# Kernel optimization log

Hardware: AMD Instinct MI355X
Metric: run time of the kernel (lower is better)

## Reference

```python
import jax, jax.numpy as jnp
import numpy as np

DIM = 2048
N_HEADS = 16
HEAD_DIM = DIM // N_HEADS        # 128
HALF_HD = HEAD_DIM // 2          # 64 (per-context per-head dim)
Q_DIM = DIM // 2                 # 1024
KV_DIM = DIM // 2                # 1024 (n_kv_heads == n_heads)
TOTAL = Q_DIM + 2 * KV_DIM       # 3072
B, S = 2, 2048
EPS = 1e-5


def rmsnorm(x, w, eps=EPS):
    return x * jax.lax.rsqrt(jnp.mean(x * x, axis=-1, keepdims=True) + eps) * w


def rope(x, freqs):
    # x: [B,S,H,D] with D even; freqs: [S, D//2] angles
    xr = x[..., 0::2]
    xi = x[..., 1::2]
    cos = jnp.cos(freqs)[None, :, None, :]
    sin = jnp.sin(freqs)[None, :, None, :]
    out_r = xr * cos - xi * sin
    out_i = xr * sin + xi * cos
    return jnp.stack([out_r, out_i], axis=-1).reshape(x.shape)


def setup_inputs() -> dict:
    key = jax.random.key(0)
    ks = jax.random.split(key, 10)
    inp = {
        "local_c": jax.random.normal(ks[0], (B, S, DIM), jnp.float32),
        "global_c": jax.random.normal(ks[1], (B, S, DIM), jnp.float32),
        "freqs": jax.random.uniform(ks[2], (S, HALF_HD // 2), jnp.float32) * 6.28,
        "W_lc": jax.random.normal(ks[3], (TOTAL, DIM), jnp.float32) * 0.02,
        "W_gc": jax.random.normal(ks[4], (TOTAL, DIM), jnp.float32) * 0.02,
        "q_lc_nw": jnp.ones((Q_DIM,), jnp.float32),
        "k_lc_nw": jnp.ones((KV_DIM,), jnp.float32),
        "q_gc_nw": jnp.ones((Q_DIM,), jnp.float32),
        "k_gc_nw": jnp.ones((KV_DIM,), jnp.float32),
        "q_cat_nw": jnp.ones((HEAD_DIM,), jnp.float32),
        "k_cat_nw": jnp.ones((HEAD_DIM,), jnp.float32),
        "W_lo": jax.random.normal(ks[5], (DIM, 2 * Q_DIM), jnp.float32) * 0.02,
        "b_lo": jnp.zeros((DIM,), jnp.float32),
        "lc_on_w": jnp.ones((DIM,), jnp.float32),
        "W_go": jax.random.normal(ks[6], (DIM, 2 * Q_DIM), jnp.float32) * 0.02,
        "b_go": jnp.zeros((DIM,), jnp.float32),
        "gc_on_w": jnp.ones((DIM,), jnp.float32),
    }
    return inp


def _context_build(x, W, q_nw, k_nw):
    comb = jnp.einsum('bsd,td->bst', x, W)
    q, k, v = jnp.split(comb, [Q_DIM, Q_DIM + KV_DIM], axis=-1)
    q = rmsnorm(q, q_nw).reshape(B, S, N_HEADS, HALF_HD)
    k = rmsnorm(k, k_nw).reshape(B, S, N_HEADS, HALF_HD)
    v = v.reshape(B, S, N_HEADS, HALF_HD)
    return q, k, v


def reference(local_c, global_c, freqs, W_lc, W_gc, q_lc_nw, k_lc_nw, q_gc_nw,
              k_gc_nw, q_cat_nw, k_cat_nw, W_lo, b_lo, lc_on_w, W_go, b_go, gc_on_w):
    q_lc, k_lc, v_lc = _context_build(local_c, W_lc, q_lc_nw, k_lc_nw)
    q_gc, k_gc, v_gc = _context_build(global_c, W_gc, q_gc_nw, k_gc_nw)

    q_lc = rope(q_lc, freqs)
    k_lc = rope(k_lc, freqs)
    q_gc = rope(q_gc, freqs)
    k_gc = rope(k_gc, freqs)

    # concat local+global per head -> [B,S,H,HEAD_DIM], QK-norm over head dim
    xq = rmsnorm(jnp.concatenate([q_lc, q_gc], axis=-1), q_cat_nw)
    xk = rmsnorm(jnp.concatenate([k_lc, k_gc], axis=-1), k_cat_nw)
    xv = jnp.concatenate([v_lc, v_gc], axis=-1)

    scale = 1.0 / np.sqrt(HEAD_DIM)
    scores = jnp.einsum('bqhd,bkhd->bhqk', xq, xk) * scale
    attn = jax.nn.softmax(scores, axis=-1)
    out = jnp.einsum('bhqk,bkhd->bqhd', attn, xv).reshape(B, S, DIM)

    x_lc = rmsnorm(jnp.einsum('bsd,od->bso', out, W_lo) + b_lo, lc_on_w)
    x_gc = rmsnorm(jnp.einsum('bsd,od->bso', out, W_go) + b_go, gc_on_w)
    return (x_lc, x_gc)
```

## Files before the change

### kernel.cpp

```cpp
#include <hip/hip_runtime.h>
#include <hip/hip_bf16.h>

#define DIM 2048
#define NH 16
#define HD 128
#define QD 1024
#define TOT 3072
#define BB 2
#define SS 2048
#define NTOK (BB*SS)
#define EPS 1e-5f

typedef __attribute__((ext_vector_type(4))) float f32x4;
typedef __attribute__((ext_vector_type(8))) short short8;
typedef __attribute__((ext_vector_type(8))) unsigned short u16x8;
typedef __attribute__((ext_vector_type(4))) unsigned short u16x4;

__device__ __forceinline__ float b2f(unsigned short u){
    unsigned int x = ((unsigned int)u) << 16;
    return __builtin_bit_cast(float, x);
}
__device__ __forceinline__ unsigned short f2b(float f){
    unsigned int x = __builtin_bit_cast(unsigned int, f);
    x = (x + 0x7fffu + ((x >> 16) & 1u)) >> 16;
    return (unsigned short)x;
}
__device__ __forceinline__ float exp2_fast(float x){
    float r;
    asm("v_exp_f32 %0, %1" : "=v"(r) : "v"(x));
    return r;
}
__device__ __forceinline__ void store_c(float* p, float v){ *p = v; }
__device__ __forceinline__ void store_c(unsigned short* p, float v){ *p = f2b(v); }

#define MFMA16(a,b,c) __builtin_amdgcn_mfma_f32_16x16x32_bf16((a),(b),(c),0,0,0)

#define GLOAD16(g, l) __builtin_amdgcn_global_load_lds( \
    (const __attribute__((address_space(1))) unsigned int*)(g), \
    (__attribute__((address_space(3))) unsigned int*)(l), 16, 0, 0)

__device__ __forceinline__ void cvt8(const float* __restrict__ s,
                                     unsigned short* __restrict__ d, int i){
    const float4* p = reinterpret_cast<const float4*>(s + (size_t)i * 8);
    float4 a = p[0], b = p[1];
    u16x8 o;
    o[0]=f2b(a.x); o[1]=f2b(a.y); o[2]=f2b(a.z); o[3]=f2b(a.w);
    o[4]=f2b(b.x); o[5]=f2b(b.y); o[6]=f2b(b.z); o[7]=f2b(b.w);
    *reinterpret_cast<u16x8*>(d + (size_t)i * 8) = o;
}

__global__ __launch_bounds__(256) void cvt_multi(
    const float* __restrict__ s0, const float* __restrict__ s1,
    const float* __restrict__ s2, const float* __restrict__ s3,
    const float* __restrict__ s4, const float* __restrict__ s5,
    unsigned short* __restrict__ d0, unsigned short* __restrict__ d1,
    unsigned short* __restrict__ d2, unsigned short* __restrict__ d3,
    unsigned short* __restrict__ d4, unsigned short* __restrict__ d5)
{
    const int N0 = NTOK*DIM/8;
    const int N1 = N0 + NTOK*DIM/8;
    const int N2 = N1 + TOT*DIM/8;
    const int N3 = N2 + TOT*DIM/8;
    const int N4 = N3 + DIM*DIM/8;
    const int N5 = N4 + DIM*DIM/8;
    for (int i = blockIdx.x * blockDim.x + threadIdx.x; i < N5;
         i += gridDim.x * blockDim.x){
        if      (i < N0) cvt8(s0, d0, i);
        else if (i < N1) cvt8(s1, d1, i - N0);
        else if (i < N2) cvt8(s2, d2, i - N1);
        else if (i < N3) cvt8(s3, d3, i - N2);
        else if (i < N4) cvt8(s4, d4, i - N3);
        else             cvt8(s5, d5, i - N4);
    }
}

template<typename OutT>
__global__ __launch_bounds__(256) void gemm_nt(const unsigned short* __restrict__ A0,
                                               const unsigned short* __restrict__ B0,
                                               OutT* __restrict__ C0,
                                               const unsigned short* __restrict__ A1,
                                               const unsigned short* __restrict__ B1,
                                               OutT* __restrict__ C1,
                                               int M, int N, int K){
    __shared__ __attribute__((aligned(16))) unsigned short As[2][128*64];
    __shared__ __attribute__((aligned(16))) unsigned short Bs[3][128*64];
    const int t = threadIdx.x;
    const int lane = t & 63;
    const int w = t >> 6;
    const int wr = w >> 1, wc = w & 1;
    const int gx = gridDim.x;
    const int nwg = gx * gridDim.y;
    int zsel, swz;
    if (gridDim.z == 2){
        const int glin = (int)(blockIdx.z * nwg + blockIdx.y * gx + blockIdx.x);
        const int xcd = glin & 7;
        const int i = glin >> 3;
        zsel = xcd >> 2;
        swz = (xcd & 3) * (nwg >> 2) + i;
    } else {
        const int lin = (int)(blockIdx.y * gx + blockIdx.x);
        const int cpx = nwg >> 3;
        swz = (lin & 7) * cpx + (lin >> 3);
        zsel = 0;
    }
    const unsigned short* A = zsel ? A1 : A0;
    const unsigned short* B = zsel ? B1 : B0;
    OutT* C = zsel ? C1 : C0;
    const int m0 = (swz / gx) * 128, n0 = (swz % gx) * 128;
    const int l16 = lane & 15, lq = lane >> 4;

    f32x4 acc[4][4];
    const f32x4 z = {0.f, 0.f, 0.f, 0.f};
    #pragma unroll
    for (int m = 0; m < 4; ++m)
        #pragma unroll
        for (int n = 0; n < 4; ++n) acc[m][n] = z;

    auto stageA = [&](int kt, int bi){
        #pragma unroll
        for (int i = 0; i < 4; ++i){
            int c = t + 256 * i;
            int row = c >> 3, c8 = c & 7;
            int cg = (c8 ^ (row & 7)) * 8;
            GLOAD16(&A[(size_t)(m0 + row) * K + kt*64 + cg],
                    (char*)&As[bi][0] + (size_t)(i * 256 + w * 64) * 16);
        }
    };
    auto stageB = [&](int kt, int bi){
        #pragma unroll
        for (int i = 0; i < 4; ++i){
            int c = t + 256 * i;
            int row = c >> 3, c8 = c & 7;
            int cg = (c8 ^ (row & 7)) * 8;
            GLOAD16(&B[(size_t)(n0 + row) * K + kt*64 + cg],
                    (char*)&Bs[bi][0] + (size_t)(i * 256 + w * 64) * 16);
        }
    };

    const int NTt = K >> 6;
    stageA(0, 0); stageB(0, 0);
    if (NTt > 1) stageB(1, 1);
    if (NTt > 1) asm volatile("s_waitcnt vmcnt(4)" ::: "memory");
    else         asm volatile("s_waitcnt vmcnt(0)" ::: "memory");
    __builtin_amdgcn_s_barrier();
    __builtin_amdgcn_sched_barrier(0);

    int a0 = 0, b0 = 0, b1 = 1, b2 = 2;
    for (int kt = 0; kt < NTt; ++kt){
        if (kt + 1 < NTt) stageA(kt + 1, a0 ^ 1);
        if (kt + 2 < NTt) stageB(kt + 2, b2);
        #pragma unroll
        for (int kk = 0; kk < 2; ++kk){
            short8 af[4], bf[4];
            #pragma unroll
            for (int m = 0; m < 4; ++m){
                int row = wr*64 + m*16 + l16;
                af[m] = *reinterpret_cast<const short8*>(
                    &As[a0][row*64 + (((kk*4 + lq) ^ (row & 7)) * 8)]);
            }
            #pragma unroll
            for (int n = 0; n < 4; ++n){
                int row = wc*64 + n*16 + l16;
                bf[n] = *reinterpret_cast<const short8*>(
                    &Bs[b0][row*64 + (((kk*4 + lq) ^ (row & 7)) * 8)]);
            }
            #pragma unroll
            for (int m = 0; m < 4; ++m)
                #pragma unroll
                for (int n = 0; n < 4; ++n)
                    acc[m][n] = MFMA16(af[m], bf[n], acc[m][n]);
        }
        if (kt + 1 < NTt){
            if (kt + 2 < NTt) asm volatile("s_waitcnt vmcnt(4)" ::: "memory");
            else              asm volatile("s_waitcnt vmcnt(0)" ::: "memory");
            __builtin_amdgcn_s_barrier();
            __builtin_amdgcn_sched_barrier(0);
        }
        a0 ^= 1;
        int tmp = b0; b0 = b1; b1 = b2; b2 = tmp;
    }
    #pragma unroll
    for (int m = 0; m < 4; ++m){
        int grow = m0 + wr*64 + m*16 + lq*4;
        #pragma unroll
        for (int n = 0; n < 4; ++n){
            int gcol = n0 + wc*64 + n*16 + l16;
            #pragma unroll
            for (int r = 0; r < 4; ++r)
                store_c(&C[(size_t)(grow + r) * N + gcol], acc[m][n][r]);
        }
    }
}

__global__ __launch_bounds__(256) void qkv_post(
    const unsigned short* __restrict__ comb_lc, const unsigned short* __restrict__ comb_gc,
    const float* __restrict__ freqs,
    const float* __restrict__ q_lc_nw, const float* __restrict__ k_lc_nw,
    const float* __restrict__ q_gc_nw, const float* __restrict__ k_gc_nw,
    const float* __restrict__ q_cat_nw, const float* __restrict__ k_cat_nw,
    unsigned short* __restrict__ xq, unsigned short* __restrict__ xk,
    unsigned short* __restrict__ xv)
{
    __shared__ float qcat[16][128];
    __shared__ float kcat[16][128];
    __shared__ float rbuf[4][4];
    const int tok = blockIdx.x;
    const int s = tok & (SS - 1);
    const unsigned short* clc = comb_lc + (size_t)tok * TOT;
    const unsigned short* cgc = comb_gc + (size_t)tok * TOT;
    const int t = threadIdx.x;
    const int lane = t & 63, w = t >> 6;

    const unsigned short* segs[4] = { clc, clc + QD, cgc, cgc + QD };
    const float* wts[4] = { q_lc_nw, k_lc_nw, q_gc_nw, k_gc_nw };

    float ss4[4];
    #pragma unroll
    for (int sg = 0; sg < 4; ++sg){
        u16x4 v = *reinterpret_cast<const u16x4*>(segs[sg] + t * 4);
        float acc = 0.f;
        #pragma unroll
        for (int j = 0; j < 4; ++j){ float f = b2f(v[j]); acc += f * f; }
        ss4[sg] = acc;
    }
    #pragma unroll
    for (int sg = 0; sg < 4; ++sg){
        float v = ss4[sg];
        #pragma unroll
        for (int o = 32; o >= 1; o >>= 1) v += __shfl_xor(v, o);
        if (lane == 0) rbuf[sg][w] = v;
    }
    __syncthreads();
    float rms[4];
    #pragma unroll
    for (int sg = 0; sg < 4; ++sg){
        float tot = rbuf[sg][0] + rbuf[sg][1] + rbuf[sg][2] + rbuf[sg][3];
        rms[sg] = rsqrtf(tot * (1.f / QD) + EPS);
    }

    #pragma unroll
    for (int sg = 0; sg < 4; ++sg){
        const unsigned short* seg = segs[sg];
        const float* wt = wts[sg];
        const float rf = rms[sg];
        float (*dst)[128] = (sg == 0 || sg == 2) ? qcat : kcat;
        const int coff = (sg >= 2) ? 64 : 0;
        #pragma unroll
        for (int pi = 0; pi < 2; ++pi){
            int p = t + pi * 256;
            int h = p >> 5, j = p & 31;
            int idx = h * 64 + 2 * j;
            float xr = b2f(seg[idx])     * rf * wt[idx];
            float xi = b2f(seg[idx + 1]) * rf * wt[idx + 1];
            float fr = freqs[(size_t)s * 32 + j];
            float cs = __cosf(fr), sn = __sinf(fr);
            dst[h][coff + 2*j]     = xr * cs - xi * sn;
            dst[h][coff + 2*j + 1] = xr * sn + xi * cs;
        }
    }

    {
        int i0 = t * 4;
        int h = i0 >> 6, d = i0 & 63;
        u16x4 vlc = *reinterpret_cast<const u16x4*>(clc + 2048 + i0);
        u16x4 vgc = *reinterpret_cast<const u16x4*>(cgc + 2048 + i0);
        *reinterpret_cast<u16x4*>(&xv[(size_t)tok * DIM + h * 128 + d])      = vlc;
        *reinterpret_cast<u16x4*>(&xv[(size_t)tok * DIM + h * 128 + 64 + d]) = vgc;
    }
    __syncthreads();

    {
        int h = t >> 4, sub = t & 15;
        float sq = 0.f, sk = 0.f;
        #pragma unroll
        for (int j = 0; j < 8; ++j){
            float a = qcat[h][sub*8 + j]; sq += a * a;
            float b = kcat[h][sub*8 + j]; sk += b * b;
        }
        #pragma unroll
        for (int o = 1; o < 16; o <<= 1){ sq += __shfl_xor(sq, o); sk += __shfl_xor(sk, o); }
        float rq = rsqrtf(sq * (1.f / 128) + EPS);
        float rk = rsqrtf(sk * (1.f / 128) + EPS);
        u16x8 oq, ok;
        #pragma unroll
        for (int j = 0; j < 8; ++j){
            int d = sub*8 + j;
            oq[j] = f2b(qcat[h][d] * rq * q_cat_nw[d]);
            ok[j] = f2b(kcat[h][d] * rk * k_cat_nw[d]);
        }
        *reinterpret_cast<u16x8*>(&xq[(size_t)tok * DIM + h * 128 + sub*8]) = oq;
        *reinterpret_cast<u16x8*>(&xk[(size_t)tok * DIM + h * 128 + sub*8]) = ok;
    }
}

__global__ __launch_bounds__(256) void transpose_v(const unsigned short* __restrict__ xv,
                                                   unsigned short* __restrict__ xvT){
    __shared__ unsigned short tile[128][129];
    const int blk = blockIdx.x;
    const int st = blk & 15;
    const int bh = blk >> 4;
    const int b = bh >> 4, h = bh & 15;
    const int t = threadIdx.x;
    const int s0 = st * 128;
    #pragma unroll
    for (int i = 0; i < 8; ++i){
        int c = t + 256 * i;
        int r = c >> 4, dc = c & 15;
        u16x8 v = *reinterpret_cast<const u16x8*>(&xv[((size_t)(b*SS + s0 + r)) * DIM + h*HD + dc*8]);
        #pragma unroll
        for (int j = 0; j < 8; ++j) tile[r][dc*8 + j] = v[j];
    }
    __syncthreads();
    #pragma unroll
    for (int i = 0; i < 8; ++i){
        int c = t + 256 * i;
        int d = c >> 4, sc = c & 15;
        u16x8 o;
        #pragma unroll
        for (int j = 0; j < 8; ++j) o[j] = tile[sc*8 + j][d];
        *reinterpret_cast<u16x8*>(&xvT[((size_t)bh * HD + d) * SS + s0 + sc*8]) = o;
    }
}

__global__ __launch_bounds__(256) void attn_fwd(const unsigned short* __restrict__ xq,
                                                const unsigned short* __restrict__ xk,
                                                const unsigned short* __restrict__ xvT,
                                                unsigned short* __restrict__ attn_out){
    __shared__ __attribute__((aligned(16))) unsigned short Kl[2][64 * 128];
    __shared__ __attribute__((aligned(16))) unsigned short Vt[2][128 * 64];
    __shared__ __attribute__((aligned(16))) unsigned short Pl[4][2][16 * 64];
    const int blk = ((int)blockIdx.x & 7) * 64 + ((int)blockIdx.x >> 3);
    const int qt = blk & 15, h = (blk >> 4) & 15, b = blk >> 8;
    const int t = threadIdx.x, lane = t & 63, w = t >> 6;
    const int l16 = lane & 15, lq = lane >> 4;
    const float scale2 = 0.12751744751f;
    const float MBIAS = 16.6f;
    const int qbase = qt * 128 + w * 32;

    short8 qf[2][4];
    #pragma unroll
    for (int g = 0; g < 2; ++g)
        #pragma unroll
        for (int ks = 0; ks < 4; ++ks)
            qf[g][ks] = *reinterpret_cast<const short8*>(
                &xq[((size_t)(b*SS + qbase + g*16 + l16)) * DIM + h*HD + ks*32 + lq*8]);

    float psum[2] = {0.f, 0.f};
    f32x4 O[2][8];
    const f32x4 z = {0.f, 0.f, 0.f, 0.f};
    #pragma unroll
    for (int g = 0; g < 2; ++g)
        #pragma unroll
        for (int dn = 0; dn < 8; ++dn) O[g][dn] = z;

    const size_t kbase = (size_t)(b*SS) * DIM + h*HD;
    const size_t vbase = ((size_t)(b*NH + h)) * HD * SS;

    auto stage = [&](int kt, int bi){
        #pragma unroll
        for (int i = 0; i < 4; ++i){
            int slot = i*256 + w*64 + lane;
            int r = slot >> 4, dc = slot & 15;
            GLOAD16(&xk[kbase + (size_t)(kt*64 + r) * DIM + ((dc ^ (r & 7)) * 8)],
                    (char*)&Kl[bi][0] + (size_t)(i*256 + w*64) * 16);
            int d = slot >> 3, kc = slot & 7;
            GLOAD16(&xvT[vbase + (size_t)d * SS + kt*64 + ((kc ^ (d & 7)) * 8)],
                    (char*)&Vt[bi][0] + (size_t)(i*256 + w*64) * 16);
        }
    };

    stage(0, 0);
    __syncthreads();

    int cur = 0;

    for (int kt = 0; kt < SS/64; ++kt){
        if (kt + 1 < SS/64) stage(kt + 1, cur ^ 1);

        const unsigned short* Kc = Kl[cur];
        const unsigned short* Vc = Vt[cur];

        #pragma unroll
        for (int g = 0; g < 2; ++g){
            f32x4 St[4];
            #pragma unroll
            for (int kn = 0; kn < 4; ++kn) St[kn] = z;
            __builtin_amdgcn_s_setprio(1);
            #pragma unroll
            for (int kn = 0; kn < 4; ++kn){
                int kr = kn*16 + l16;
                #pragma unroll
                for (int ks = 0; ks < 4; ++ks){
                    short8 ak = *reinterpret_cast<const short8*>(
                        &Kc[kr*128 + (((ks*4 + lq) ^ (kr & 7)) * 8)]);
                    St[kn] = MFMA16(ak, qf[g][ks], St[kn]);
                }
            }
            __builtin_amdgcn_s_setprio(0);

            unsigned short* P = Pl[w][g];
            #pragma unroll
            for (int kn = 0; kn < 4; ++kn){
                float p0 = exp2_fast(St[kn][0]*scale2 - MBIAS);
                float p1 = exp2_fast(St[kn][1]*scale2 - MBIAS);
                float p2 = exp2_fast(St[kn][2]*scale2 - MBIAS);
                float p3 = exp2_fast(St[kn][3]*scale2 - MBIAS);
                psum[g] += (p0 + p1) + (p2 + p3);
                unsigned lo, hi;
                asm("v_cvt_pk_bf16_f32 %0, %1, %2" : "=v"(lo) : "v"(p0), "v"(p1));
                asm("v_cvt_pk_bf16_f32 %0, %1, %2" : "=v"(hi) : "v"(p2), "v"(p3));
                uint2 pk2; pk2.x = lo; pk2.y = hi;
                int kk = kn >> 1;
                int lqp = (kn & 1)*2 + (lq >> 1);
                *reinterpret_cast<uint2*>(&P[(kk*64 + lqp*16 + l16)*8 + (lq & 1)*4]) = pk2;
            }
        }
        asm volatile("s_waitcnt lgkmcnt(0)" ::: "memory");
        __builtin_amdgcn_sched_barrier(0);

        __builtin_amdgcn_s_setprio(1);
        #pragma unroll
        for (int kk = 0; kk < 2; ++kk){
            short8 pb0 = *reinterpret_cast<const short8*>(&Pl[w][0][(kk*64 + lq*16 + l16)*8]);
            short8 pb1 = *reinterpret_cast<const short8*>(&Pl[w][1][(kk*64 + lq*16 + l16)*8]);
            #pragma unroll
            for (int dn = 0; dn < 8; ++dn){
                int dr = dn*16 + l16;
                short8 av = *reinterpret_cast<const short8*>(
                    &Vc[dr*64 + (((kk*4 + lq) ^ (dr & 7)) * 8)]);
                O[0][dn] = MFMA16(av, pb0, O[0][dn]);
                O[1][dn] = MFMA16(av, pb1, O[1][dn]);
            }
        }
        __builtin_amdgcn_s_setprio(0);

        __syncthreads();
        cur ^= 1;
    }

    #pragma unroll
    for (int g = 0; g < 2; ++g){
        float ps = psum[g];
        ps += __shfl_xor(ps, 16);
        ps += __shfl_xor(ps, 32);
        float inv = 1.f / ps;
        #pragma unroll
        for (int dn = 0; dn < 8; ++dn){
            u16x4 o4;
            #pragma unroll
            for (int r = 0; r < 4; ++r) o4[r] = f2b(O[g][dn][r] * inv);
            *reinterpret_cast<u16x4*>(
                &attn_out[((size_t)(b*SS + qbase + g*16 + l16)) * DIM + h*HD + dn*16 + lq*4]) = o4;
        }
    }
}

__global__ __launch_bounds__(256) void proj_norm2(const unsigned short* __restrict__ proj,
                                                  const float* __restrict__ b_lo,
                                                  const float* __restrict__ b_go,
                                                  const float* __restrict__ w_lc,
                                                  const float* __restrict__ w_gc,
                                                  float* __restrict__ out){
    __shared__ float buf[DIM];
    __shared__ float rbuf[4];
    const int half = blockIdx.x >> 12;
    const int row  = blockIdx.x & (NTOK - 1);
    const unsigned short* p = proj + (size_t)row * (2*DIM) + (size_t)half * DIM;
    const float* bias = half ? b_go : b_lo;
    const float* w    = half ? w_gc : w_lc;
    float* o = out + (size_t)half * NTOK * DIM + (size_t)row * DIM;
    const int t = threadIdx.x;
    const int lane = t & 63, wv = t >> 6;
    float ssq = 0.f;
    #pragma unroll
    for (int i = 0; i < 8; ++i){
        int c = t + i * 256;
        float v = b2f(p[c]) + bias[c];
        buf[c] = v;
        ssq += v * v;
    }
    #pragma unroll
    for (int o2 = 32; o2 >= 1; o2 >>= 1) ssq += __shfl_xor(ssq, o2);
    if (lane == 0) rbuf[wv] = ssq;
    __syncthreads();
    float tot = rbuf[0] + rbuf[1] + rbuf[2] + rbuf[3];
    float rr = rsqrtf(tot * (1.f / DIM) + EPS);
    #pragma unroll
    for (int i = 0; i < 8; ++i){
        int c = t + i * 256;
        o[c] = buf[c] * rr * w[c];
    }
}

extern "C" void kernel_launch(void* const* d_in, const int* in_sizes, int n_in,
                              void* d_out, int out_size, void* d_ws, size_t ws_size,
                              hipStream_t stream)
{
    const float* local_c  = (const float*)d_in[0];
    const float* global_c = (const float*)d_in[1];
    const float* freqs    = (const float*)d_in[2];
    const float* W_lc     = (const float*)d_in[3];
    const float* W_gc     = (const float*)d_in[4];
    const float* q_lc_nw  = (const float*)d_in[5];
    const float* k_lc_nw  = (const float*)d_in[6];
    const float* q_gc_nw  = (const float*)d_in[7];
    const float* k_gc_nw  = (const float*)d_in[8];
    const float* q_cat_nw = (const float*)d_in[9];
    const float* k_cat_nw = (const float*)d_in[10];
    const float* W_lo     = (const float*)d_in[11];
    const float* b_lo     = (const float*)d_in[12];
    const float* lc_on_w  = (const float*)d_in[13];
    const float* W_go     = (const float*)d_in[14];
    const float* b_go     = (const float*)d_in[15];
    const float* gc_on_w  = (const float*)d_in[16];
    float* out = (float*)d_out;

    char* ws = (char*)d_ws;
    const size_t SZ_WLO  = (size_t)DIM * DIM * 2;
    const size_t SZ_WLC  = (size_t)TOT * DIM * 2;
    const size_t SZ_TOK2 = (size_t)NTOK * DIM * 2;
    const size_t SZ_COMB = (size_t)NTOK * TOT * 2;

    unsigned short* Wlo_b  = (unsigned short*)(ws);
    unsigned short* Wgo_b  = (unsigned short*)(ws + SZ_WLO);
    char*           slotW  = ws + 2*SZ_WLO;
    unsigned short* Wlc_b  = (unsigned short*)(slotW);
    unsigned short* Wgc_b  = (unsigned short*)(slotW + SZ_WLC);
    unsigned short* xv     = (unsigned short*)(slotW);
    char*           slotE  = ws + 2*SZ_WLO + 2*SZ_WLC;
    char*           slotF  = slotE + SZ_TOK2;
    unsigned short* xb_lc  = (unsigned short*)slotE;
    unsigned short* xb_gc  = (unsigned short*)slotF;
    unsigned short* xq     = (unsigned short*)slotE;
    unsigned short* xk     = (unsigned short*)slotF;
    unsigned short* proj   = (unsigned short*)slotE;
    char*           slotG  = slotF + SZ_TOK2;
    char*           slotH  = slotG + SZ_COMB;
    unsigned short* comb_lc= (unsigned short*)slotG;
    unsigned short* comb_gc= (unsigned short*)slotH;
    unsigned short* xvT    = (unsigned short*)slotG;
    unsigned short* attn_o = (unsigned short*)slotH;
    (void)ws_size;

    cvt_multi<<<2048, 256, 0, stream>>>(local_c, global_c, W_lc, W_gc, W_lo, W_go,
                                        xb_lc, xb_gc, Wlc_b, Wgc_b, Wlo_b, Wgo_b);

    dim3 g1(TOT / 128, NTOK / 128, 2);
    gemm_nt<unsigned short><<<g1, 256, 0, stream>>>(xb_lc, Wlc_b, comb_lc,
                                                    xb_gc, Wgc_b, comb_gc, NTOK, TOT, DIM);

    qkv_post<<<NTOK, 256, 0, stream>>>(comb_lc, comb_gc, freqs,
                                       q_lc_nw, k_lc_nw, q_gc_nw, k_gc_nw,
                                       q_cat_nw, k_cat_nw, xq, xk, xv);

    transpose_v<<<512, 256, 0, stream>>>(xv, xvT);

    attn_fwd<<<512, 256, 0, stream>>>(xq, xk, xvT, attn_o);

    dim3 g2(2 * DIM / 128, NTOK / 128, 1);
    gemm_nt<unsigned short><<<g2, 256, 0, stream>>>(attn_o, Wlo_b, proj,
                                                    attn_o, Wlo_b, proj, NTOK, 2*DIM, DIM);

    proj_norm2<<<2*NTOK, 256, 0, stream>>>(proj, b_lo, b_go, lc_on_w, gc_on_w, out);
}
```

Before: 373.4 us.

## Replace 128x128 GEMM with 256x256-tile 8-wave kernel with interleaved prefetch

```diff
diff --git a/kernel.cpp b/kernel.cpp
--- a/kernel.cpp
+++ b/kernel.cpp
@@ -30,8 +30,6 @@
     asm("v_exp_f32 %0, %1" : "=v"(r) : "v"(x));
     return r;
 }
-__device__ __forceinline__ void store_c(float* p, float v){ *p = v; }
-__device__ __forceinline__ void store_c(unsigned short* p, float v){ *p = f2b(v); }
 
 #define MFMA16(a,b,c) __builtin_amdgcn_mfma_f32_16x16x32_bf16((a),(b),(c),0,0,0)
 
@@ -74,20 +72,18 @@
     }
 }
 
-template<typename OutT>
-__global__ __launch_bounds__(256) void gemm_nt(const unsigned short* __restrict__ A0,
-                                               const unsigned short* __restrict__ B0,
-                                               OutT* __restrict__ C0,
-                                               const unsigned short* __restrict__ A1,
-                                               const unsigned short* __restrict__ B1,
-                                               OutT* __restrict__ C1,
-                                               int M, int N, int K){
-    __shared__ __attribute__((aligned(16))) unsigned short As[2][128*64];
-    __shared__ __attribute__((aligned(16))) unsigned short Bs[3][128*64];
+__global__ __launch_bounds__(512, 2) void gemm256(
+    const unsigned short* __restrict__ A0, const unsigned short* __restrict__ B0,
+    unsigned short* __restrict__ C0,
+    const unsigned short* __restrict__ A1, const unsigned short* __restrict__ B1,
+    unsigned short* __restrict__ C1, int M, int N, int K)
+{
+    __shared__ __attribute__((aligned(16))) unsigned short LA[2][2][128*64];
+    __shared__ __attribute__((aligned(16))) unsigned short LB[2][2][128*64];
     const int t = threadIdx.x;
-    const int lane = t & 63;
-    const int w = t >> 6;
-    const int wr = w >> 1, wc = w & 1;
+    const int lane = t & 63, w = t >> 6;
+    const int wr = w >> 2, wc = w & 3;
+    const int l16 = lane & 15, lq = lane >> 4;
     const int gx = gridDim.x;
     const int nwg = gx * gridDim.y;
     int zsel, swz;
@@ -99,95 +95,114 @@
         swz = (xcd & 3) * (nwg >> 2) + i;
     } else {
         const int lin = (int)(blockIdx.y * gx + blockIdx.x);
-        const int cpx = nwg >> 3;
-        swz = (lin & 7) * cpx + (lin >> 3);
+        swz = (lin & 7) * (nwg >> 3) + (lin >> 3);
         zsel = 0;
     }
     const unsigned short* A = zsel ? A1 : A0;
     const unsigned short* B = zsel ? B1 : B0;
-    OutT* C = zsel ? C1 : C0;
-    const int m0 = (swz / gx) * 128, n0 = (swz % gx) * 128;
-    const int l16 = lane & 15, lq = lane >> 4;
-
-    f32x4 acc[4][4];
+    unsigned short* C = zsel ? C1 : C0;
+    const int m0 = (swz / gx) * 256, n0 = (swz % gx) * 256;
+
+    f32x4 acc[8][4];
     const f32x4 z = {0.f, 0.f, 0.f, 0.f};
     #pragma unroll
-    for (int m = 0; m < 4; ++m)
-        #pragma unroll
-        for (int n = 0; n < 4; ++n) acc[m][n] = z;
-
-    auto stageA = [&](int kt, int bi){
-        #pragma unroll
-        for (int i = 0; i < 4; ++i){
-            int c = t + 256 * i;
-            int row = c >> 3, c8 = c & 7;
-            int cg = (c8 ^ (row & 7)) * 8;
-            GLOAD16(&A[(size_t)(m0 + row) * K + kt*64 + cg],
-                    (char*)&As[bi][0] + (size_t)(i * 256 + w * 64) * 16);
-        }
+    for (int a = 0; a < 8; ++a)
+        #pragma unroll
+        for (int n = 0; n < 4; ++n) acc[a][n] = z;
+
+    auto part = [&](const unsigned short* S, int rowbase, int kt, int j2, unsigned short* slab){
+        int row = j2*64 + (t >> 3);
+        int ch  = t & 7;
+        GLOAD16(&S[(size_t)(rowbase + row) * K + kt*64 + ((ch ^ (row & 7)) * 8)],
+                (char*)slab + (size_t)(j2*512 + w*64) * 16);
     };
-    auto stageB = [&](int kt, int bi){
-        #pragma unroll
-        for (int i = 0; i < 4; ++i){
-            int c = t + 256 * i;
-            int row = c >> 3, c8 = c & 7;
-            int cg = (c8 ^ (row & 7)) * 8;
-            GLOAD16(&B[(size_t)(n0 + row) * K + kt*64 + cg],
-                    (char*)&Bs[bi][0] + (size_t)(i * 256 + w * 64) * 16);
-        }
-    };
-
-    const int NTt = K >> 6;
-    stageA(0, 0); stageB(0, 0);
-    if (NTt > 1) stageB(1, 1);
-    if (NTt > 1) asm volatile("s_waitcnt vmcnt(4)" ::: "memory");
-    else         asm volatile("s_waitcnt vmcnt(0)" ::: "memory");
+
+    const int NT = K >> 6;
+    part(B, n0+0,   0, 0, &LB[0][0][0]); part(B, n0+0,   0, 1, &LB[0][0][0]);
+    part(B, n0+128, 0, 0, &LB[0][1][0]); part(B, n0+128, 0, 1, &LB[0][1][0]);
+    part(A, m0+0,   0, 0, &LA[0][0][0]); part(A, m0+128, 0, 0, &LA[0][1][0]);
+    part(A, m0+0,   0, 1, &LA[0][0][0]); part(A, m0+128, 0, 1, &LA[0][1][0]);
+    if (NT > 1){
+        part(B, n0+0,   1, 0, &LB[1][0][0]); part(B, n0+0,   1, 1, &LB[1][0][0]);
+        part(A, m0+0,   1, 0, &LA[1][0][0]); part(A, m0+128, 1, 0, &LA[1][1][0]);
+        part(B, n0+128, 1, 0, &LB[1][1][0]); part(B, n0+128, 1, 1, &LB[1][1][0]);
+        asm volatile("s_waitcnt vmcnt(6)" ::: "memory");
+    } else {
+        asm volatile("s_waitcnt vmcnt(0)" ::: "memory");
+    }
     __builtin_amdgcn_s_barrier();
+    asm volatile("" ::: "memory");
     __builtin_amdgcn_sched_barrier(0);
 
-    int a0 = 0, b0 = 0, b1 = 1, b2 = 2;
-    for (int kt = 0; kt < NTt; ++kt){
-        if (kt + 1 < NTt) stageA(kt + 1, a0 ^ 1);
-        if (kt + 2 < NTt) stageB(kt + 2, b2);
-        #pragma unroll
-        for (int kk = 0; kk < 2; ++kk){
-            short8 af[4], bf[4];
-            #pragma unroll
-            for (int m = 0; m < 4; ++m){
-                int row = wr*64 + m*16 + l16;
-                af[m] = *reinterpret_cast<const short8*>(
-                    &As[a0][row*64 + (((kk*4 + lq) ^ (row & 7)) * 8)]);
-            }
-            #pragma unroll
-            for (int n = 0; n < 4; ++n){
-                int row = wc*64 + n*16 + l16;
-                bf[n] = *reinterpret_cast<const short8*>(
-                    &Bs[b0][row*64 + (((kk*4 + lq) ^ (row & 7)) * 8)]);
-            }
-            #pragma unroll
-            for (int m = 0; m < 4; ++m)
+    for (int kt = 0; kt < NT; ++kt){
+        const int pc = kt & 1;
+        const int p1 = pc ^ 1;
+        short8 bfr[4][2];
+        #pragma unroll
+        for (int q = 0; q < 4; ++q){
+            if (q == 0 && kt + 1 < NT){
+                part(A, m0+0,   kt+1, 1, &LA[p1][0][0]);
+                part(A, m0+128, kt+1, 1, &LA[p1][1][0]);
+            }
+            if (q == 1 && kt + 2 < NT){
+                part(B, n0+0,   kt+2, 0, &LB[pc][0][0]);
+                part(B, n0+0,   kt+2, 1, &LB[pc][0][0]);
+            }
+            if (q == 2 && kt + 2 < NT){
+                part(A, m0+0,   kt+2, 0, &LA[pc][0][0]);
+                part(A, m0+128, kt+2, 0, &LA[pc][1][0]);
+            }
+            if (q == 3 && kt + 2 < NT){
+                part(B, n0+128, kt+2, 0, &LB[pc][1][0]);
+                part(B, n0+128, kt+2, 1, &LB[pc][1][0]);
+            }
+            short8 afr[2][2];
+            #pragma unroll
+            for (int mi = 0; mi < 2; ++mi){
+                int lr = q*32 + mi*16 + l16;
                 #pragma unroll
-                for (int n = 0; n < 4; ++n)
-                    acc[m][n] = MFMA16(af[m], bf[n], acc[m][n]);
-        }
-        if (kt + 1 < NTt){
-            if (kt + 2 < NTt) asm volatile("s_waitcnt vmcnt(4)" ::: "memory");
-            else              asm volatile("s_waitcnt vmcnt(0)" ::: "memory");
+                for (int kk = 0; kk < 2; ++kk)
+                    afr[mi][kk] = *reinterpret_cast<const short8*>(
+                        &LA[pc][wr][lr*64 + (((kk*4 + lq) ^ (lr & 7)) * 8)]);
+            }
+            if (q == 0){
+                #pragma unroll
+                for (int n = 0; n < 4; ++n){
+                    int lb = (wc & 1)*64 + n*16 + l16;
+                    #pragma unroll
+                    for (int kk = 0; kk < 2; ++kk)
+                        bfr[n][kk] = *reinterpret_cast<const short8*>(
+                            &LB[pc][wc >> 1][lb*64 + (((kk*4 + lq) ^ (lb & 7)) * 8)]);
+                }
+            }
+            __builtin_amdgcn_s_setprio(1);
+            #pragma unroll
+            for (int kk = 0; kk < 2; ++kk)
+                #pragma unroll
+                for (int mi = 0; mi < 2; ++mi)
+                    #pragma unroll
+                    for (int n = 0; n < 4; ++n)
+                        acc[q*2 + mi][n] = MFMA16(afr[mi][kk], bfr[n][kk], acc[q*2 + mi][n]);
+            __builtin_amdgcn_s_setprio(0);
+            if (q == 3 && kt + 1 < NT){
+                if (kt + 2 < NT) asm volatile("s_waitcnt vmcnt(6)" ::: "memory");
+                else             asm volatile("s_waitcnt vmcnt(0)" ::: "memory");
+            }
             __builtin_amdgcn_s_barrier();
+            asm volatile("" ::: "memory");
             __builtin_amdgcn_sched_barrier(0);
         }
-        a0 ^= 1;
-        int tmp = b0; b0 = b1; b1 = b2; b2 = tmp;
-    }
-    #pragma unroll
-    for (int m = 0; m < 4; ++m){
-        int grow = m0 + wr*64 + m*16 + lq*4;
+    }
+
+    #pragma unroll
+    for (int a = 0; a < 8; ++a){
+        int grow = m0 + wr*128 + (a >> 1)*32 + (a & 1)*16 + lq*4;
         #pragma unroll
         for (int n = 0; n < 4; ++n){
             int gcol = n0 + wc*64 + n*16 + l16;
             #pragma unroll
             for (int r = 0; r < 4; ++r)
-                store_c(&C[(size_t)(grow + r) * N + gcol], acc[m][n][r]);
+                C[(size_t)(grow + r) * N + gcol] = f2b(acc[a][n][r]);
         }
     }
 }
@@ -545,9 +560,9 @@
     cvt_multi<<<2048, 256, 0, stream>>>(local_c, global_c, W_lc, W_gc, W_lo, W_go,
                                         xb_lc, xb_gc, Wlc_b, Wgc_b, Wlo_b, Wgo_b);
 
-    dim3 g1(TOT / 128, NTOK / 128, 2);
-    gemm_nt<unsigned short><<<g1, 256, 0, stream>>>(xb_lc, Wlc_b, comb_lc,
-                                                    xb_gc, Wgc_b, comb_gc, NTOK, TOT, DIM);
+    dim3 g1(TOT / 256, NTOK / 256, 2);
+    gemm256<<<g1, 512, 0, stream>>>(xb_lc, Wlc_b, comb_lc,
+                                    xb_gc, Wgc_b, comb_gc, NTOK, TOT, DIM);
 
     qkv_post<<<NTOK, 256, 0, stream>>>(comb_lc, comb_gc, freqs,
                                        q_lc_nw, k_lc_nw, q_gc_nw, k_gc_nw,
@@ -557,9 +572,9 @@
 
     attn_fwd<<<512, 256, 0, stream>>>(xq, xk, xvT, attn_o);
 
-    dim3 g2(2 * DIM / 128, NTOK / 128, 1);
-    gemm_nt<unsigned short><<<g2, 256, 0, stream>>>(attn_o, Wlo_b, proj,
-                                                    attn_o, Wlo_b, proj, NTOK, 2*DIM, DIM);
+    dim3 g2(2 * DIM / 256, NTOK / 256, 1);
+    gemm256<<<g2, 512, 0, stream>>>(attn_o, Wlo_b, proj,
+                                    attn_o, Wlo_b, proj, NTOK, 2*DIM, DIM);
 
     proj_norm2<<<2*NTOK, 256, 0, stream>>>(proj, b_lo, b_go, lc_on_w, gc_on_w, out);
 }
```

After: 372.4 us. No clear change (-0.3%).
